# Kernel optimization log

Hardware: AMD Instinct MI355X
Metric: run time of the kernel (lower is better)

The kernel has to match this reference:

```python
import jax, jax.numpy as jnp
import numpy as np

N_NODES = 100000
N_EDGES = 3200000
IN_DIM = 128


def setup_inputs() -> dict:
    key = jax.random.key(0)
    ks = jax.random.split(key, 6)
    x = jax.random.normal(ks[0], (N_NODES, IN_DIM), dtype=jnp.float32)
    edge_index = jax.random.randint(ks[1], (2, N_EDGES), 0, N_NODES, dtype=jnp.int64)
    # Glorot-ish init for weights, zero bias (PyG GCNConv default has bias)
    W1 = jax.random.normal(ks[2], (IN_DIM, 32), dtype=jnp.float32) / np.sqrt(IN_DIM)
    b1 = jnp.zeros((32,), dtype=jnp.float32)
    W2 = jax.random.normal(ks[3], (32, 16), dtype=jnp.float32) / np.sqrt(32.0)
    b2 = jnp.zeros((16,), dtype=jnp.float32)
    Wf = jax.random.normal(ks[4], (16, 1), dtype=jnp.float32) / np.sqrt(16.0)
    bf = jnp.zeros((1,), dtype=jnp.float32)
    return {"x": x, "edge_index": edge_index, "W1": W1, "b1": b1,
            "W2": W2, "b2": b2, "Wf": Wf, "bf": bf}


def reference(x, edge_index, W1, b1, W2, b2, Wf, bf):
    N = x.shape[0]
    # PyG GCNConv: add self-loops, symmetric normalization D^-1/2 (A+I) D^-1/2
    loop = jnp.arange(N, dtype=edge_index.dtype)
    src = jnp.concatenate([edge_index[0], loop])  # message sources (x_j)
    dst = jnp.concatenate([edge_index[1], loop])  # aggregation targets
    deg = jax.ops.segment_sum(jnp.ones_like(dst, dtype=x.dtype), dst, num_segments=N)
    dinv = jax.lax.rsqrt(jnp.maximum(deg, 1.0))  # deg >= 1 due to self-loops
    norm = dinv[src] * dinv[dst]                  # per-edge coefficient

    def gcn_conv(h, W, b):
        h = h @ W                                 # linear transform first (small dim)
        msg = h[src] * norm[:, None]              # gather + scale
        return jax.ops.segment_sum(msg, dst, num_segments=N) + b  # scatter-add

    h = jax.nn.relu(gcn_conv(x, W1, b1))
    h = jax.nn.relu(gcn_conv(h, W2, b2))
    return (h @ Wf + bf).squeeze(-1)              # [N]
```

## Files before the change

### kernel.cpp

```cpp
#include <hip/hip_runtime.h>


#define TPB 256
#define NBUCK 512
#define BCAP 8192
#define CHUNK 8192

__device__ __forceinline__ unsigned f2bf(float f) {
    unsigned u = __float_as_uint(f);
    return (u + 0x7FFFu + ((u >> 16) & 1u)) >> 16;
}
__device__ __forceinline__ float bflo(unsigned u) { return __uint_as_float(u << 16); }
__device__ __forceinline__ float bfhi(unsigned u) { return __uint_as_float(u & 0xFFFF0000u); }

__global__ __launch_bounds__(512) void binA2_kernel(
        const int* __restrict__ src, const int* __restrict__ dst,
        int* __restrict__ bcur, unsigned* __restrict__ staging, int E, int NPB) {
    __shared__ unsigned packed[CHUNK];
    __shared__ unsigned short buckb[CHUNK];
    __shared__ int hist[NBUCK];
    __shared__ int scan_[NBUCK];
    __shared__ int lstart[NBUCK];
    __shared__ int lcur[NBUCK];
    __shared__ int gbase[NBUCK];
    int tid = threadIdx.x;
    int start = blockIdx.x * CHUNK;
    int sz = min(CHUNK, E - start);

    if (tid < NBUCK) hist[tid] = 0;
    __syncthreads();
    for (int i = tid; i < sz; i += 512) {
        unsigned d = (unsigned)dst[start + i];
        atomicAdd(&hist[d / (unsigned)NPB], 1);
    }
    __syncthreads();
    int v = (tid < NBUCK) ? hist[tid] : 0;
    if (tid < NBUCK) scan_[tid] = v;
    __syncthreads();
    for (int dd = 1; dd < NBUCK; dd <<= 1) {
        int t = 0;
        if (tid < NBUCK && tid >= dd) t = scan_[tid - dd];
        __syncthreads();
        if (tid < NBUCK) scan_[tid] += t;
        __syncthreads();
    }
    if (tid < NBUCK) {
        lstart[tid] = scan_[tid] - v;
        lcur[tid] = 0;
        gbase[tid] = atomicAdd(&bcur[tid], v);
    }
    __syncthreads();
    for (int i = tid; i < sz; i += 512) {
        unsigned d = (unsigned)dst[start + i];
        unsigned s = (unsigned)src[start + i];
        unsigned b = d / (unsigned)NPB;
        unsigned loc = d - b * (unsigned)NPB;
        int pos = atomicAdd(&lcur[b], 1);
        int si = lstart[b] + pos;
        packed[si] = (loc << 20) | s;
        buckb[si] = (unsigned short)b;
    }
    __syncthreads();
    for (int i = tid; i < sz; i += 512) {
        unsigned b = buckb[i];
        int dsti = gbase[b] + (i - lstart[b]);
        if (dsti < BCAP)
            staging[(size_t)b * BCAP + dsti] = packed[i];
    }
}

__global__ void buildB_kernel(const int* __restrict__ bcur,
                              const unsigned* __restrict__ staging,
                              int* __restrict__ offs, int* __restrict__ counts,
                              float* __restrict__ dinv, int* __restrict__ csr_src,
                              int N, int NPB) {
    __shared__ int sb[NBUCK];
    __shared__ int hist[512];
    __shared__ int scan_[512];
    __shared__ int cur[512];
    int b = blockIdx.x;
    int tid = threadIdx.x;
    if (tid < NBUCK) sb[tid] = min(bcur[tid], BCAP);
    __syncthreads();
    for (int d = 1; d < NBUCK; d <<= 1) {
        int t = 0;
        if (tid < NBUCK && tid >= d) t = sb[tid - d];
        __syncthreads();
        if (tid < NBUCK) sb[tid] += t;
        __syncthreads();
    }
    int sz = min(bcur[b], BCAP);
    int base = (b == 0) ? 0 : sb[b - 1];
    int n0 = b * NPB;
    int nn = min(NPB, N - n0);
    const unsigned* se = staging + (size_t)b * BCAP;

    hist[tid] = 0;
    __syncthreads();
    for (int i = tid; i < sz; i += 512)
        atomicAdd(&hist[se[i] >> 20], 1);
    __syncthreads();
    int h = hist[tid];
    scan_[tid] = h;
    __syncthreads();
    for (int d = 1; d < 512; d <<= 1) {
        int t = 0;
        if (tid >= d) t = scan_[tid - d];
        __syncthreads();
        scan_[tid] += t;
        __syncthreads();
    }
    int excl = scan_[tid] - h;
    cur[tid] = excl;
    if (tid < nn) {
        int node = n0 + tid;
        offs[node] = base + excl;
        counts[node] = h;
        dinv[node] = rsqrtf((float)(h + 1));
    }
    __syncthreads();
    for (int i = tid; i < sz; i += 512) {
        unsigned p = se[i];
        int pos = atomicAdd(&cur[p >> 20], 1);
        csr_src[base + pos] = (int)(p & 0xFFFFFu);
    }
}

__global__ __launch_bounds__(256) void gemm1_kernel(
        const float* __restrict__ x, const float* __restrict__ W1,
        const float* __restrict__ dinv, unsigned* __restrict__ xwd, int N) {
    __shared__ float ws_[128 * 32];
    for (int i = threadIdx.x; i < 128 * 32; i += 256) ws_[i] = W1[i];
    __syncthreads();
    int t = threadIdx.x;
    int jq = (t & 3) * 8;
    int n0 = blockIdx.x * 256 + (t >> 2) * 4;
    if (n0 >= N) return;
    int nc0 = min(n0 + 0, N - 1);
    int nc1 = min(n0 + 1, N - 1);
    int nc2 = min(n0 + 2, N - 1);
    int nc3 = min(n0 + 3, N - 1);
    const float4* xr0 = (const float4*)(x + (size_t)nc0 * 128);
    const float4* xr1 = (const float4*)(x + (size_t)nc1 * 128);
    const float4* xr2 = (const float4*)(x + (size_t)nc2 * 128);
    const float4* xr3 = (const float4*)(x + (size_t)nc3 * 128);
    float acc[4][8];
#pragma unroll
    for (int n = 0; n < 4; ++n)
#pragma unroll
        for (int j = 0; j < 8; ++j) acc[n][j] = 0.0f;
#pragma unroll 2
    for (int k4 = 0; k4 < 32; ++k4) {
        const float* wb = ws_ + (k4 * 4) * 32 + jq;
        float4 a0 = *(const float4*)(wb);
        float4 a1 = *(const float4*)(wb + 4);
        float4 b0 = *(const float4*)(wb + 32);
        float4 b1v = *(const float4*)(wb + 36);
        float4 c0 = *(const float4*)(wb + 64);
        float4 c1 = *(const float4*)(wb + 68);
        float4 d0 = *(const float4*)(wb + 96);
        float4 d1 = *(const float4*)(wb + 100);
        float4 xv0 = xr0[k4];
        float4 xv1 = xr1[k4];
        float4 xv2 = xr2[k4];
        float4 xv3 = xr3[k4];
#pragma unroll
        for (int n = 0; n < 4; ++n) {
            float4 xv = (n == 0) ? xv0 : (n == 1) ? xv1 : (n == 2) ? xv2 : xv3;
            acc[n][0] += xv.x * a0.x + xv.y * b0.x + xv.z * c0.x + xv.w * d0.x;
            acc[n][1] += xv.x * a0.y + xv.y * b0.y + xv.z * c0.y + xv.w * d0.y;
            acc[n][2] += xv.x * a0.z + xv.y * b0.z + xv.z * c0.z + xv.w * d0.z;
            acc[n][3] += xv.x * a0.w + xv.y * b0.w + xv.z * c0.w + xv.w * d0.w;
            acc[n][4] += xv.x * a1.x + xv.y * b1v.x + xv.z * c1.x + xv.w * d1.x;
            acc[n][5] += xv.x * a1.y + xv.y * b1v.y + xv.z * c1.y + xv.w * d1.y;
            acc[n][6] += xv.x * a1.z + xv.y * b1v.z + xv.z * c1.z + xv.w * d1.z;
            acc[n][7] += xv.x * a1.w + xv.y * b1v.w + xv.z * c1.w + xv.w * d1.w;
        }
    }
#pragma unroll
    for (int n = 0; n < 4; ++n) {
        int node = n0 + n;
        if (node >= N) break;
        float d = dinv[node];
        unsigned pk0 = f2bf(acc[n][0] * d) | (f2bf(acc[n][1] * d) << 16);
        unsigned pk1 = f2bf(acc[n][2] * d) | (f2bf(acc[n][3] * d) << 16);
        unsigned pk2 = f2bf(acc[n][4] * d) | (f2bf(acc[n][5] * d) << 16);
        unsigned pk3 = f2bf(acc[n][6] * d) | (f2bf(acc[n][7] * d) << 16);
        ((uint4*)(xwd + (size_t)node * 16))[t & 3] = make_uint4(pk0, pk1, pk2, pk3);
    }
}

__global__ __launch_bounds__(256) void aggF_kernel(
        const int* __restrict__ offs, const int* __restrict__ counts,
        const int* __restrict__ csr_src, const float* __restrict__ dinv,
        const unsigned* __restrict__ xwd, const float* __restrict__ b1,
        const float* __restrict__ W2, unsigned* __restrict__ h2wd, int N) {
    __shared__ float ws2[32 * 16];
    for (int i = threadIdx.x; i < 512; i += 256) ws2[i] = W2[i];
    __syncthreads();
    int t = threadIdx.x;
    int q = t & 3;
    int node = blockIdx.x * 64 + (t >> 2);
    if (node >= N) return;
    int off = offs[node];
    int deg = counts[node];
    float acc[8];
    {
        uint4 v = ((const uint4*)(xwd + (size_t)node * 16))[q];
        acc[0] = bflo(v.x); acc[1] = bfhi(v.x);
        acc[2] = bflo(v.y); acc[3] = bfhi(v.y);
        acc[4] = bflo(v.z); acc[5] = bfhi(v.z);
        acc[6] = bflo(v.w); acc[7] = bfhi(v.w);
    }
    int i = 0;
    for (; i + 1 < deg; i += 2) {
        int s0 = csr_src[off + i];
        int s1 = csr_src[off + i + 1];
        uint4 v0 = ((const uint4*)(xwd + (size_t)s0 * 16))[q];
        uint4 v1 = ((const uint4*)(xwd + (size_t)s1 * 16))[q];
        acc[0] += bflo(v0.x) + bflo(v1.x); acc[1] += bfhi(v0.x) + bfhi(v1.x);
        acc[2] += bflo(v0.y) + bflo(v1.y); acc[3] += bfhi(v0.y) + bfhi(v1.y);
        acc[4] += bflo(v0.z) + bflo(v1.z); acc[5] += bfhi(v0.z) + bfhi(v1.z);
        acc[6] += bflo(v0.w) + bflo(v1.w); acc[7] += bfhi(v0.w) + bfhi(v1.w);
    }
    if (i < deg) {
        int s = csr_src[off + i];
        uint4 v = ((const uint4*)(xwd + (size_t)s * 16))[q];
        acc[0] += bflo(v.x); acc[1] += bfhi(v.x);
        acc[2] += bflo(v.y); acc[3] += bfhi(v.y);
        acc[4] += bflo(v.z); acc[5] += bfhi(v.z);
        acc[6] += bflo(v.w); acc[7] += bfhi(v.w);
    }
    float dv = dinv[node];
    float part[16];
#pragma unroll
    for (int j = 0; j < 16; ++j) part[j] = 0.0f;
    const float* bq = b1 + q * 8;
#pragma unroll
    for (int k = 0; k < 8; ++k) {
        float h = fmaxf(acc[k] * dv + bq[k], 0.0f);
        const float* wr = ws2 + (q * 8 + k) * 16;
        float4 w0 = *(const float4*)(wr);
        float4 w1 = *(const float4*)(wr + 4);
        float4 w2 = *(const float4*)(wr + 8);
        float4 w3 = *(const float4*)(wr + 12);
        part[0]  += h * w0.x; part[1]  += h * w0.y; part[2]  += h * w0.z; part[3]  += h * w0.w;
        part[4]  += h * w1.x; part[5]  += h * w1.y; part[6]  += h * w1.z; part[7]  += h * w1.w;
        part[8]  += h * w2.x; part[9]  += h * w2.y; part[10] += h * w2.z; part[11] += h * w2.w;
        part[12] += h * w3.x; part[13] += h * w3.y; part[14] += h * w3.z; part[15] += h * w3.w;
    }
    float p8[8];
#pragma unroll
    for (int j = 0; j < 8; ++j) {
        float send = (q & 1) ? part[j] : part[j + 8];
        float keep = (q & 1) ? part[j + 8] : part[j];
        p8[j] = keep + __shfl_xor(send, 1, 64);
    }
    float p4[4];
#pragma unroll
    for (int j = 0; j < 4; ++j) {
        float send = (q & 2) ? p8[j] : p8[j + 4];
        float keep = (q & 2) ? p8[j + 4] : p8[j];
        p4[j] = keep + __shfl_xor(send, 2, 64);
    }
    unsigned pk0 = f2bf(p4[0] * dv) | (f2bf(p4[1] * dv) << 16);
    unsigned pk1 = f2bf(p4[2] * dv) | (f2bf(p4[3] * dv) << 16);
    int slot = ((q & 1) << 1) | ((q >> 1) & 1);
    ((uint2*)(h2wd + (size_t)node * 8))[slot] = make_uint2(pk0, pk1);
}

__global__ __launch_bounds__(256) void aggS16f_kernel(
        const int* __restrict__ offs, const int* __restrict__ counts,
        const int* __restrict__ csr_src, const float* __restrict__ dinv,
        const unsigned* __restrict__ h2wd,
        const float* __restrict__ b2, const float* __restrict__ Wf,
        const float* __restrict__ bf, float* __restrict__ out, int N) {
    __shared__ float bs_[16];
    __shared__ float wf_[16];
    __shared__ float bfv;
    int t = threadIdx.x;
    if (t < 16) { bs_[t] = b2[t]; wf_[t] = Wf[t]; }
    if (t == 0) bfv = bf[0];
    __syncthreads();
    int q = t & 1;
    int node = blockIdx.x * 128 + (t >> 1);
    if (node >= N) return;
    int off = offs[node];
    int deg = counts[node];
    float acc[8];
    {
        uint4 v = ((const uint4*)(h2wd + (size_t)node * 8))[q];
        acc[0] = bflo(v.x); acc[1] = bfhi(v.x);
        acc[2] = bflo(v.y); acc[3] = bfhi(v.y);
        acc[4] = bflo(v.z); acc[5] = bfhi(v.z);
        acc[6] = bflo(v.w); acc[7] = bfhi(v.w);
    }
    int i = 0;
    for (; i + 1 < deg; i += 2) {
        int s0 = csr_src[off + i];
        int s1 = csr_src[off + i + 1];
        uint4 v0 = ((const uint4*)(h2wd + (size_t)s0 * 8))[q];
        uint4 v1 = ((const uint4*)(h2wd + (size_t)s1 * 8))[q];
        acc[0] += bflo(v0.x) + bflo(v1.x); acc[1] += bfhi(v0.x) + bfhi(v1.x);
        acc[2] += bflo(v0.y) + bflo(v1.y); acc[3] += bfhi(v0.y) + bfhi(v1.y);
        acc[4] += bflo(v0.z) + bflo(v1.z); acc[5] += bfhi(v0.z) + bfhi(v1.z);
        acc[6] += bflo(v0.w) + bflo(v1.w); acc[7] += bfhi(v0.w) + bfhi(v1.w);
    }
    if (i < deg) {
        int s = csr_src[off + i];
        uint4 v = ((const uint4*)(h2wd + (size_t)s * 8))[q];
        acc[0] += bflo(v.x); acc[1] += bfhi(v.x);
        acc[2] += bflo(v.y); acc[3] += bfhi(v.y);
        acc[4] += bflo(v.z); acc[5] += bfhi(v.z);
        acc[6] += bflo(v.w); acc[7] += bfhi(v.w);
    }
    float dv = dinv[node];
    const float* bq = bs_ + q * 8;
    const float* wq = wf_ + q * 8;
    float part = 0.f;
#pragma unroll
    for (int k = 0; k < 8; ++k)
        part += fmaxf(acc[k] * dv + bq[k], 0.f) * wq[k];
    part += __shfl_xor(part, 1, 64);
    if (q == 0) out[node] = part + bfv;
}

extern "C" void kernel_launch(void* const* d_in, const int* in_sizes, int n_in,
                              void* d_out, int out_size, void* d_ws, size_t ws_size,
                              hipStream_t stream) {
    const float* x  = (const float*)d_in[0];
    const int*   ei = (const int*)d_in[1];
    const float* W1 = (const float*)d_in[2];
    const float* b1 = (const float*)d_in[3];
    const float* W2 = (const float*)d_in[4];
    const float* b2 = (const float*)d_in[5];
    const float* Wf = (const float*)d_in[6];
    const float* bf = (const float*)d_in[7];

    int N = in_sizes[0] / 128;
    int E = in_sizes[1] / 2;
    const int* src = ei;
    const int* dst = ei + E;
    int NPB = (N + NBUCK - 1) / NBUCK;

    size_t Np = ((size_t)N + 3) & ~(size_t)3;
    size_t Ep = ((size_t)E + 3) & ~(size_t)3;
    int* wsI      = (int*)d_ws;
    int* counts   = wsI;
    int* offs     = counts + Np;
    int* bcur     = offs + Np;
    int* csr_src  = bcur + NBUCK;
    float* dinv   = (float*)(csr_src + Ep);
    unsigned* xwd = (unsigned*)(dinv + Np);
    unsigned* staging = xwd + 16 * Np;
    unsigned* h2wd = staging;
    float* out    = (float*)d_out;

    int nbG1 = (N + 255) / 256;
    int nbC  = (E + CHUNK - 1) / CHUNK;
    int nbA32 = (N + 63) / 64;
    int nbA16 = (N + 127) / 128;

    hipMemsetAsync(bcur, 0, NBUCK * sizeof(int), stream);
    binA2_kernel<<<nbC, 512, 0, stream>>>(src, dst, bcur, staging, E, NPB);
    buildB_kernel<<<NBUCK, 512, 0, stream>>>(bcur, staging, offs, counts,
                                             dinv, csr_src, N, NPB);
    gemm1_kernel<<<nbG1, 256, 0, stream>>>(x, W1, dinv, xwd, N);
    aggF_kernel<<<nbA32, 256, 0, stream>>>(offs, counts, csr_src, dinv, xwd,
                                           b1, W2, h2wd, N);
    aggS16f_kernel<<<nbA16, 256, 0, stream>>>(offs, counts, csr_src, dinv, h2wd,
                                              b2, Wf, bf, out, N);
}
```

Measured before the change: 259.6 us.

## Aggregate directly from destination buckets with shared-memory atomics, dropping CSR build

Result: slower. 1.004 ms (+286.6%).

```diff
diff --git a/kernel.cpp b/kernel.cpp
--- a/kernel.cpp
+++ b/kernel.cpp
@@ -1,10 +1,10 @@
 #include <hip/hip_runtime.h>
 
 
-#define TPB 256
 #define NBUCK 512
 #define BCAP 8192
-#define CHUNK 8192
+#define CHUNK 4096
+#define NPBMAX 256
 
 __device__ __forceinline__ unsigned f2bf(float f) {
     unsigned u = __float_as_uint(f);
@@ -27,37 +27,45 @@
     int start = blockIdx.x * CHUNK;
     int sz = min(CHUNK, E - start);
 
-    if (tid < NBUCK) hist[tid] = 0;
-    __syncthreads();
-    for (int i = tid; i < sz; i += 512) {
-        unsigned d = (unsigned)dst[start + i];
-        atomicAdd(&hist[d / (unsigned)NPB], 1);
-    }
-    __syncthreads();
-    int v = (tid < NBUCK) ? hist[tid] : 0;
-    if (tid < NBUCK) scan_[tid] = v;
+    unsigned dreg[8], sreg[8];
+    hist[tid] = 0;
+#pragma unroll
+    for (int c = 0; c < 8; ++c) {
+        int i = tid + c * 512;
+        if (i < sz) {
+            dreg[c] = (unsigned)dst[start + i];
+            sreg[c] = (unsigned)src[start + i];
+        } else {
+            dreg[c] = 0xFFFFFFFFu;
+        }
+    }
+    __syncthreads();
+#pragma unroll
+    for (int c = 0; c < 8; ++c)
+        if (dreg[c] != 0xFFFFFFFFu) atomicAdd(&hist[dreg[c] / (unsigned)NPB], 1);
+    __syncthreads();
+    int v = hist[tid];
+    scan_[tid] = v;
     __syncthreads();
     for (int dd = 1; dd < NBUCK; dd <<= 1) {
-        int t = 0;
-        if (tid < NBUCK && tid >= dd) t = scan_[tid - dd];
+        int t = (tid >= dd) ? scan_[tid - dd] : 0;
         __syncthreads();
-        if (tid < NBUCK) scan_[tid] += t;
+        scan_[tid] += t;
         __syncthreads();
     }
-    if (tid < NBUCK) {
-        lstart[tid] = scan_[tid] - v;
-        lcur[tid] = 0;
-        gbase[tid] = atomicAdd(&bcur[tid], v);
-    }
-    __syncthreads();
-    for (int i = tid; i < sz; i += 512) {
-        unsigned d = (unsigned)dst[start + i];
-        unsigned s = (unsigned)src[start + i];
+    lstart[tid] = scan_[tid] - v;
+    lcur[tid] = 0;
+    gbase[tid] = atomicAdd(&bcur[tid], v);
+    __syncthreads();
+#pragma unroll
+    for (int c = 0; c < 8; ++c) {
+        if (dreg[c] == 0xFFFFFFFFu) continue;
+        unsigned d = dreg[c];
         unsigned b = d / (unsigned)NPB;
         unsigned loc = d - b * (unsigned)NPB;
         int pos = atomicAdd(&lcur[b], 1);
         int si = lstart[b] + pos;
-        packed[si] = (loc << 20) | s;
+        packed[si] = (loc << 20) | sreg[c];
         buckb[si] = (unsigned short)b;
     }
     __syncthreads();
@@ -69,61 +77,22 @@
     }
 }
 
-__global__ void buildB_kernel(const int* __restrict__ bcur,
-                              const unsigned* __restrict__ staging,
-                              int* __restrict__ offs, int* __restrict__ counts,
-                              float* __restrict__ dinv, int* __restrict__ csr_src,
-                              int N, int NPB) {
-    __shared__ int sb[NBUCK];
-    __shared__ int hist[512];
-    __shared__ int scan_[512];
-    __shared__ int cur[512];
+__global__ __launch_bounds__(512) void countB_kernel(
+        const int* __restrict__ bcur, const unsigned* __restrict__ staging,
+        float* __restrict__ dinv, int N, int NPB) {
+    __shared__ int hist[NPBMAX];
     int b = blockIdx.x;
     int tid = threadIdx.x;
-    if (tid < NBUCK) sb[tid] = min(bcur[tid], BCAP);
-    __syncthreads();
-    for (int d = 1; d < NBUCK; d <<= 1) {
-        int t = 0;
-        if (tid < NBUCK && tid >= d) t = sb[tid - d];
-        __syncthreads();
-        if (tid < NBUCK) sb[tid] += t;
-        __syncthreads();
-    }
+    if (tid < NPBMAX) hist[tid] = 0;
+    __syncthreads();
     int sz = min(bcur[b], BCAP);
-    int base = (b == 0) ? 0 : sb[b - 1];
-    int n0 = b * NPB;
-    int nn = min(NPB, N - n0);
     const unsigned* se = staging + (size_t)b * BCAP;
-
-    hist[tid] = 0;
-    __syncthreads();
     for (int i = tid; i < sz; i += 512)
         atomicAdd(&hist[se[i] >> 20], 1);
     __syncthreads();
-    int h = hist[tid];
-    scan_[tid] = h;
-    __syncthreads();
-    for (int d = 1; d < 512; d <<= 1) {
-        int t = 0;
-        if (tid >= d) t = scan_[tid - d];
-        __syncthreads();
-        scan_[tid] += t;
-        __syncthreads();
-    }
-    int excl = scan_[tid] - h;
-    cur[tid] = excl;
-    if (tid < nn) {
-        int node = n0 + tid;
-        offs[node] = base + excl;
-        counts[node] = h;
-        dinv[node] = rsqrtf((float)(h + 1));
-    }
-    __syncthreads();
-    for (int i = tid; i < sz; i += 512) {
-        unsigned p = se[i];
-        int pos = atomicAdd(&cur[p >> 20], 1);
-        csr_src[base + pos] = (int)(p & 0xFFFFFu);
-    }
+    int n0 = b * NPB;
+    if (tid < NPB && n0 + tid < N)
+        dinv[n0 + tid] = rsqrtf((float)(hist[tid] + 1));
 }
 
 __global__ __launch_bounds__(256) void gemm1_kernel(
@@ -190,139 +159,121 @@
     }
 }
 
-__global__ __launch_bounds__(256) void aggF_kernel(
-        const int* __restrict__ offs, const int* __restrict__ counts,
-        const int* __restrict__ csr_src, const float* __restrict__ dinv,
-        const unsigned* __restrict__ xwd, const float* __restrict__ b1,
-        const float* __restrict__ W2, unsigned* __restrict__ h2wd, int N) {
+__global__ __launch_bounds__(512) void aggB1_kernel(
+        const int* __restrict__ bcur, const unsigned* __restrict__ staging,
+        const float* __restrict__ dinv, const unsigned* __restrict__ xwd,
+        const float* __restrict__ b1, const float* __restrict__ W2,
+        unsigned* __restrict__ h2wd, int N, int NPB) {
+    __shared__ float acc[NPBMAX * 33];
     __shared__ float ws2[32 * 16];
-    for (int i = threadIdx.x; i < 512; i += 256) ws2[i] = W2[i];
-    __syncthreads();
-    int t = threadIdx.x;
-    int q = t & 3;
-    int node = blockIdx.x * 64 + (t >> 2);
-    if (node >= N) return;
-    int off = offs[node];
-    int deg = counts[node];
-    float acc[8];
-    {
-        uint4 v = ((const uint4*)(xwd + (size_t)node * 16))[q];
-        acc[0] = bflo(v.x); acc[1] = bfhi(v.x);
-        acc[2] = bflo(v.y); acc[3] = bfhi(v.y);
-        acc[4] = bflo(v.z); acc[5] = bfhi(v.z);
-        acc[6] = bflo(v.w); acc[7] = bfhi(v.w);
-    }
-    int i = 0;
-    for (; i + 1 < deg; i += 2) {
-        int s0 = csr_src[off + i];
-        int s1 = csr_src[off + i + 1];
-        uint4 v0 = ((const uint4*)(xwd + (size_t)s0 * 16))[q];
-        uint4 v1 = ((const uint4*)(xwd + (size_t)s1 * 16))[q];
-        acc[0] += bflo(v0.x) + bflo(v1.x); acc[1] += bfhi(v0.x) + bfhi(v1.x);
-        acc[2] += bflo(v0.y) + bflo(v1.y); acc[3] += bfhi(v0.y) + bfhi(v1.y);
-        acc[4] += bflo(v0.z) + bflo(v1.z); acc[5] += bfhi(v0.z) + bfhi(v1.z);
-        acc[6] += bflo(v0.w) + bflo(v1.w); acc[7] += bfhi(v0.w) + bfhi(v1.w);
-    }
-    if (i < deg) {
-        int s = csr_src[off + i];
+    __shared__ float bs1[32];
+    int b = blockIdx.x;
+    int tid = threadIdx.x;
+    int n0 = b * NPB;
+    int nn = min(NPB, N - n0);
+    if (nn <= 0) return;
+    if (tid < 512) ws2[tid] = W2[tid];
+    if (tid < 32) bs1[tid] = b1[tid];
+    for (int i = tid; i < nn * 4; i += 512) {
+        int loc = i >> 2, q = i & 3;
+        uint4 v = ((const uint4*)(xwd + (size_t)(n0 + loc) * 16))[q];
+        float* a = acc + loc * 33 + q * 8;
+        a[0] = bflo(v.x); a[1] = bfhi(v.x);
+        a[2] = bflo(v.y); a[3] = bfhi(v.y);
+        a[4] = bflo(v.z); a[5] = bfhi(v.z);
+        a[6] = bflo(v.w); a[7] = bfhi(v.w);
+    }
+    __syncthreads();
+    int sz = min(bcur[b], BCAP);
+    const unsigned* se = staging + (size_t)b * BCAP;
+    int q = tid & 3;
+    for (int e = tid >> 2; e < sz; e += 128) {
+        unsigned p = se[e];
+        int loc = p >> 20;
+        int s = (int)(p & 0xFFFFFu);
         uint4 v = ((const uint4*)(xwd + (size_t)s * 16))[q];
-        acc[0] += bflo(v.x); acc[1] += bfhi(v.x);
-        acc[2] += bflo(v.y); acc[3] += bfhi(v.y);
-        acc[4] += bflo(v.z); acc[5] += bfhi(v.z);
-        acc[6] += bflo(v.w); acc[7] += bfhi(v.w);
-    }
-    float dv = dinv[node];
-    float part[16];
-#pragma unroll
-    for (int j = 0; j < 16; ++j) part[j] = 0.0f;
-    const float* bq = b1 + q * 8;
-#pragma unroll
-    for (int k = 0; k < 8; ++k) {
-        float h = fmaxf(acc[k] * dv + bq[k], 0.0f);
-        const float* wr = ws2 + (q * 8 + k) * 16;
-        float4 w0 = *(const float4*)(wr);
-        float4 w1 = *(const float4*)(wr + 4);
-        float4 w2 = *(const float4*)(wr + 8);
-        float4 w3 = *(const float4*)(wr + 12);
-        part[0]  += h * w0.x; part[1]  += h * w0.y; part[2]  += h * w0.z; part[3]  += h * w0.w;
-        part[4]  += h * w1.x; part[5]  += h * w1.y; part[6]  += h * w1.z; part[7]  += h * w1.w;
-        part[8]  += h * w2.x; part[9]  += h * w2.y; part[10] += h * w2.z; part[11] += h * w2.w;
-        part[12] += h * w3.x; part[13] += h * w3.y; part[14] += h * w3.z; part[15] += h * w3.w;
-    }
-    float p8[8];
-#pragma unroll
-    for (int j = 0; j < 8; ++j) {
-        float send = (q & 1) ? part[j] : part[j + 8];
-        float keep = (q & 1) ? part[j + 8] : part[j];
-        p8[j] = keep + __shfl_xor(send, 1, 64);
-    }
-    float p4[4];
-#pragma unroll
-    for (int j = 0; j < 4; ++j) {
-        float send = (q & 2) ? p8[j] : p8[j + 4];
-        float keep = (q & 2) ? p8[j + 4] : p8[j];
-        p4[j] = keep + __shfl_xor(send, 2, 64);
-    }
-    unsigned pk0 = f2bf(p4[0] * dv) | (f2bf(p4[1] * dv) << 16);
-    unsigned pk1 = f2bf(p4[2] * dv) | (f2bf(p4[3] * dv) << 16);
-    int slot = ((q & 1) << 1) | ((q >> 1) & 1);
-    ((uint2*)(h2wd + (size_t)node * 8))[slot] = make_uint2(pk0, pk1);
-}
-
-__global__ __launch_bounds__(256) void aggS16f_kernel(
-        const int* __restrict__ offs, const int* __restrict__ counts,
-        const int* __restrict__ csr_src, const float* __restrict__ dinv,
-        const unsigned* __restrict__ h2wd,
+        float* a = acc + loc * 33 + q * 8;
+        atomicAdd(&a[0], bflo(v.x)); atomicAdd(&a[1], bfhi(v.x));
+        atomicAdd(&a[2], bflo(v.y)); atomicAdd(&a[3], bfhi(v.y));
+        atomicAdd(&a[4], bflo(v.z)); atomicAdd(&a[5], bfhi(v.z));
+        atomicAdd(&a[6], bflo(v.w)); atomicAdd(&a[7], bfhi(v.w));
+    }
+    __syncthreads();
+    for (int loc = tid; loc < nn; loc += 512) {
+        int node = n0 + loc;
+        float dv = dinv[node];
+        const float* a = acc + loc * 33;
+        float h[32];
+#pragma unroll
+        for (int k = 0; k < 32; ++k) h[k] = fmaxf(a[k] * dv + bs1[k], 0.0f);
+        float o[16];
+#pragma unroll
+        for (int j = 0; j < 16; ++j) o[j] = 0.0f;
+#pragma unroll
+        for (int k = 0; k < 32; ++k) {
+            float hv = h[k];
+#pragma unroll
+            for (int j = 0; j < 16; ++j) o[j] += hv * ws2[k * 16 + j];
+        }
+        unsigned pk[8];
+#pragma unroll
+        for (int j = 0; j < 8; ++j)
+            pk[j] = f2bf(o[2 * j] * dv) | (f2bf(o[2 * j + 1] * dv) << 16);
+        uint4* hp = (uint4*)(h2wd + (size_t)node * 8);
+        hp[0] = make_uint4(pk[0], pk[1], pk[2], pk[3]);
+        hp[1] = make_uint4(pk[4], pk[5], pk[6], pk[7]);
+    }
+}
+
+__global__ __launch_bounds__(512) void aggB2_kernel(
+        const int* __restrict__ bcur, const unsigned* __restrict__ staging,
+        const float* __restrict__ dinv, const unsigned* __restrict__ h2wd,
         const float* __restrict__ b2, const float* __restrict__ Wf,
-        const float* __restrict__ bf, float* __restrict__ out, int N) {
-    __shared__ float bs_[16];
-    __shared__ float wf_[16];
-    __shared__ float bfv;
-    int t = threadIdx.x;
-    if (t < 16) { bs_[t] = b2[t]; wf_[t] = Wf[t]; }
-    if (t == 0) bfv = bf[0];
-    __syncthreads();
-    int q = t & 1;
-    int node = blockIdx.x * 128 + (t >> 1);
-    if (node >= N) return;
-    int off = offs[node];
-    int deg = counts[node];
-    float acc[8];
-    {
-        uint4 v = ((const uint4*)(h2wd + (size_t)node * 8))[q];
-        acc[0] = bflo(v.x); acc[1] = bfhi(v.x);
-        acc[2] = bflo(v.y); acc[3] = bfhi(v.y);
-        acc[4] = bflo(v.z); acc[5] = bfhi(v.z);
-        acc[6] = bflo(v.w); acc[7] = bfhi(v.w);
-    }
-    int i = 0;
-    for (; i + 1 < deg; i += 2) {
-        int s0 = csr_src[off + i];
-        int s1 = csr_src[off + i + 1];
-        uint4 v0 = ((const uint4*)(h2wd + (size_t)s0 * 8))[q];
-        uint4 v1 = ((const uint4*)(h2wd + (size_t)s1 * 8))[q];
-        acc[0] += bflo(v0.x) + bflo(v1.x); acc[1] += bfhi(v0.x) + bfhi(v1.x);
-        acc[2] += bflo(v0.y) + bflo(v1.y); acc[3] += bfhi(v0.y) + bfhi(v1.y);
-        acc[4] += bflo(v0.z) + bflo(v1.z); acc[5] += bfhi(v0.z) + bfhi(v1.z);
-        acc[6] += bflo(v0.w) + bflo(v1.w); acc[7] += bfhi(v0.w) + bfhi(v1.w);
-    }
-    if (i < deg) {
-        int s = csr_src[off + i];
+        const float* __restrict__ bfp, float* __restrict__ out, int N, int NPB) {
+    __shared__ float acc[NPBMAX * 17];
+    __shared__ float bs2[16];
+    __shared__ float wf[16];
+    int b = blockIdx.x;
+    int tid = threadIdx.x;
+    int n0 = b * NPB;
+    int nn = min(NPB, N - n0);
+    if (nn <= 0) return;
+    if (tid < 16) { bs2[tid] = b2[tid]; wf[tid] = Wf[tid]; }
+    for (int i = tid; i < nn * 2; i += 512) {
+        int loc = i >> 1, q = i & 1;
+        uint4 v = ((const uint4*)(h2wd + (size_t)(n0 + loc) * 8))[q];
+        float* a = acc + loc * 17 + q * 8;
+        a[0] = bflo(v.x); a[1] = bfhi(v.x);
+        a[2] = bflo(v.y); a[3] = bfhi(v.y);
+        a[4] = bflo(v.z); a[5] = bfhi(v.z);
+        a[6] = bflo(v.w); a[7] = bfhi(v.w);
+    }
+    __syncthreads();
+    int sz = min(bcur[b], BCAP);
+    const unsigned* se = staging + (size_t)b * BCAP;
+    int q = tid & 1;
+    for (int e = tid >> 1; e < sz; e += 256) {
+        unsigned p = se[e];
+        int loc = p >> 20;
+        int s = (int)(p & 0xFFFFFu);
         uint4 v = ((const uint4*)(h2wd + (size_t)s * 8))[q];
-        acc[0] += bflo(v.x); acc[1] += bfhi(v.x);
-        acc[2] += bflo(v.y); acc[3] += bfhi(v.y);
-        acc[4] += bflo(v.z); acc[5] += bfhi(v.z);
-        acc[6] += bflo(v.w); acc[7] += bfhi(v.w);
-    }
-    float dv = dinv[node];
-    const float* bq = bs_ + q * 8;
-    const float* wq = wf_ + q * 8;
-    float part = 0.f;
-#pragma unroll
-    for (int k = 0; k < 8; ++k)
-        part += fmaxf(acc[k] * dv + bq[k], 0.f) * wq[k];
-    part += __shfl_xor(part, 1, 64);
-    if (q == 0) out[node] = part + bfv;
+        float* a = acc + loc * 17 + q * 8;
+        atomicAdd(&a[0], bflo(v.x)); atomicAdd(&a[1], bfhi(v.x));
+        atomicAdd(&a[2], bflo(v.y)); atomicAdd(&a[3], bfhi(v.y));
+        atomicAdd(&a[4], bflo(v.z)); atomicAdd(&a[5], bfhi(v.z));
+        atomicAdd(&a[6], bflo(v.w)); atomicAdd(&a[7], bfhi(v.w));
+    }
+    __syncthreads();
+    for (int loc = tid; loc < nn; loc += 512) {
+        int node = n0 + loc;
+        float dv = dinv[node];
+        const float* a = acc + loc * 17;
+        float part = 0.0f;
+#pragma unroll
+        for (int k = 0; k < 16; ++k)
+            part += fmaxf(a[k] * dv + bs2[k], 0.0f) * wf[k];
+        out[node] = part + bfp[0];
+    }
 }
 
 extern "C" void kernel_launch(void* const* d_in, const int* in_sizes, int n_in,
@@ -344,30 +295,22 @@
     int NPB = (N + NBUCK - 1) / NBUCK;
 
     size_t Np = ((size_t)N + 3) & ~(size_t)3;
-    size_t Ep = ((size_t)E + 3) & ~(size_t)3;
-    int* wsI      = (int*)d_ws;
-    int* counts   = wsI;
-    int* offs     = counts + Np;
-    int* bcur     = offs + Np;
-    int* csr_src  = bcur + NBUCK;
-    float* dinv   = (float*)(csr_src + Ep);
-    unsigned* xwd = (unsigned*)(dinv + Np);
-    unsigned* staging = xwd + 16 * Np;
-    unsigned* h2wd = staging;
-    float* out    = (float*)d_out;
-
+    int* bcur        = (int*)d_ws;
+    float* dinv      = (float*)(bcur + NBUCK);
+    unsigned* xwd    = (unsigned*)(dinv + Np);
+    unsigned* h2wd   = xwd + 16 * Np;
+    unsigned* staging= h2wd + 8 * Np;
+    float* out       = (float*)d_out;
+
+    int nbC  = (E + CHUNK - 1) / CHUNK;
     int nbG1 = (N + 255) / 256;
-    int nbC  = (E + CHUNK - 1) / CHUNK;
-    int nbA32 = (N + 63) / 64;
-    int nbA16 = (N + 127) / 128;
 
     hipMemsetAsync(bcur, 0, NBUCK * sizeof(int), stream);
     binA2_kernel<<<nbC, 512, 0, stream>>>(src, dst, bcur, staging, E, NPB);
-    buildB_kernel<<<NBUCK, 512, 0, stream>>>(bcur, staging, offs, counts,
-                                             dinv, csr_src, N, NPB);
+    countB_kernel<<<NBUCK, 512, 0, stream>>>(bcur, staging, dinv, N, NPB);
     gemm1_kernel<<<nbG1, 256, 0, stream>>>(x, W1, dinv, xwd, N);
-    aggF_kernel<<<nbA32, 256, 0, stream>>>(offs, counts, csr_src, dinv, xwd,
-                                           b1, W2, h2wd, N);
-    aggS16f_kernel<<<nbA16, 256, 0, stream>>>(offs, counts, csr_src, dinv, h2wd,
-                                              b2, Wf, bf, out, N);
-}
+    aggB1_kernel<<<NBUCK, 512, 0, stream>>>(bcur, staging, dinv, xwd,
+                                            b1, W2, h2wd, N, NPB);
+    aggB2_kernel<<<NBUCK, 512, 0, stream>>>(bcur, staging, dinv, h2wd,
+                                            b2, Wf, bf, out, N, NPB);
+}
```

## Replace bucketed two-pass CSR build with global atomic count, scan, scatter

Applied to the files above, without the earlier changes.

Measured after the change: 616.8 us. 138% more time.

```diff
diff --git a/kernel.cpp b/kernel.cpp
--- a/kernel.cpp
+++ b/kernel.cpp
@@ -2,9 +2,6 @@
 
 
 #define TPB 256
-#define NBUCK 512
-#define BCAP 8192
-#define CHUNK 8192
 
 __device__ __forceinline__ unsigned f2bf(float f) {
     unsigned u = __float_as_uint(f);
@@ -13,116 +10,69 @@
 __device__ __forceinline__ float bflo(unsigned u) { return __uint_as_float(u << 16); }
 __device__ __forceinline__ float bfhi(unsigned u) { return __uint_as_float(u & 0xFFFF0000u); }
 
-__global__ __launch_bounds__(512) void binA2_kernel(
+__global__ __launch_bounds__(256) void countA_kernel(
+        const int* __restrict__ dst, int* __restrict__ counts, int E) {
+    int stride = gridDim.x * 256;
+    for (int i = blockIdx.x * 256 + threadIdx.x; i < E; i += stride)
+        atomicAdd(&counts[dst[i]], 1);
+}
+
+__global__ __launch_bounds__(512) void scan1_kernel(
+        const int* __restrict__ counts, int* __restrict__ offs,
+        int* __restrict__ bsum, float* __restrict__ dinv, int N) {
+    __shared__ int s[512];
+    int tid = threadIdx.x;
+    int g = blockIdx.x * 512 + tid;
+    int c = (g < N) ? counts[g] : 0;
+    s[tid] = c;
+    __syncthreads();
+    for (int d = 1; d < 512; d <<= 1) {
+        int t = (tid >= d) ? s[tid - d] : 0;
+        __syncthreads();
+        s[tid] += t;
+        __syncthreads();
+    }
+    if (g < N) {
+        offs[g] = s[tid] - c;
+        dinv[g] = rsqrtf((float)(c + 1));
+    }
+    if (tid == 511) bsum[blockIdx.x] = s[511];
+}
+
+__global__ __launch_bounds__(512) void scan2_kernel(int* __restrict__ bsum, int nb) {
+    __shared__ int s[512];
+    int tid = threadIdx.x;
+    int v = (tid < nb) ? bsum[tid] : 0;
+    s[tid] = v;
+    __syncthreads();
+    for (int d = 1; d < 512; d <<= 1) {
+        int t = (tid >= d) ? s[tid - d] : 0;
+        __syncthreads();
+        s[tid] += t;
+        __syncthreads();
+    }
+    if (tid < nb) bsum[tid] = s[tid] - v;
+}
+
+__global__ __launch_bounds__(256) void scan3_kernel(
+        int* __restrict__ offs, const int* __restrict__ bsum,
+        int* __restrict__ cursor, int N) {
+    int g = blockIdx.x * 256 + threadIdx.x;
+    if (g < N) {
+        int o = offs[g] + bsum[g >> 9];
+        offs[g] = o;
+        cursor[g] = o;
+    }
+}
+
+__global__ __launch_bounds__(256) void scatter_kernel(
         const int* __restrict__ src, const int* __restrict__ dst,
-        int* __restrict__ bcur, unsigned* __restrict__ staging, int E, int NPB) {
-    __shared__ unsigned packed[CHUNK];
-    __shared__ unsigned short buckb[CHUNK];
-    __shared__ int hist[NBUCK];
-    __shared__ int scan_[NBUCK];
-    __shared__ int lstart[NBUCK];
-    __shared__ int lcur[NBUCK];
-    __shared__ int gbase[NBUCK];
-    int tid = threadIdx.x;
-    int start = blockIdx.x * CHUNK;
-    int sz = min(CHUNK, E - start);
-
-    if (tid < NBUCK) hist[tid] = 0;
-    __syncthreads();
-    for (int i = tid; i < sz; i += 512) {
-        unsigned d = (unsigned)dst[start + i];
-        atomicAdd(&hist[d / (unsigned)NPB], 1);
-    }
-    __syncthreads();
-    int v = (tid < NBUCK) ? hist[tid] : 0;
-    if (tid < NBUCK) scan_[tid] = v;
-    __syncthreads();
-    for (int dd = 1; dd < NBUCK; dd <<= 1) {
-        int t = 0;
-        if (tid < NBUCK && tid >= dd) t = scan_[tid - dd];
-        __syncthreads();
-        if (tid < NBUCK) scan_[tid] += t;
-        __syncthreads();
-    }
-    if (tid < NBUCK) {
-        lstart[tid] = scan_[tid] - v;
-        lcur[tid] = 0;
-        gbase[tid] = atomicAdd(&bcur[tid], v);
-    }
-    __syncthreads();
-    for (int i = tid; i < sz; i += 512) {
-        unsigned d = (unsigned)dst[start + i];
-        unsigned s = (unsigned)src[start + i];
-        unsigned b = d / (unsigned)NPB;
-        unsigned loc = d - b * (unsigned)NPB;
-        int pos = atomicAdd(&lcur[b], 1);
-        int si = lstart[b] + pos;
-        packed[si] = (loc << 20) | s;
-        buckb[si] = (unsigned short)b;
-    }
-    __syncthreads();
-    for (int i = tid; i < sz; i += 512) {
-        unsigned b = buckb[i];
-        int dsti = gbase[b] + (i - lstart[b]);
-        if (dsti < BCAP)
-            staging[(size_t)b * BCAP + dsti] = packed[i];
-    }
-}
-
-__global__ void buildB_kernel(const int* __restrict__ bcur,
-                              const unsigned* __restrict__ staging,
-                              int* __restrict__ offs, int* __restrict__ counts,
-                              float* __restrict__ dinv, int* __restrict__ csr_src,
-                              int N, int NPB) {
-    __shared__ int sb[NBUCK];
-    __shared__ int hist[512];
-    __shared__ int scan_[512];
-    __shared__ int cur[512];
-    int b = blockIdx.x;
-    int tid = threadIdx.x;
-    if (tid < NBUCK) sb[tid] = min(bcur[tid], BCAP);
-    __syncthreads();
-    for (int d = 1; d < NBUCK; d <<= 1) {
-        int t = 0;
-        if (tid < NBUCK && tid >= d) t = sb[tid - d];
-        __syncthreads();
-        if (tid < NBUCK) sb[tid] += t;
-        __syncthreads();
-    }
-    int sz = min(bcur[b], BCAP);
-    int base = (b == 0) ? 0 : sb[b - 1];
-    int n0 = b * NPB;
-    int nn = min(NPB, N - n0);
-    const unsigned* se = staging + (size_t)b * BCAP;
-
-    hist[tid] = 0;
-    __syncthreads();
-    for (int i = tid; i < sz; i += 512)
-        atomicAdd(&hist[se[i] >> 20], 1);
-    __syncthreads();
-    int h = hist[tid];
-    scan_[tid] = h;
-    __syncthreads();
-    for (int d = 1; d < 512; d <<= 1) {
-        int t = 0;
-        if (tid >= d) t = scan_[tid - d];
-        __syncthreads();
-        scan_[tid] += t;
-        __syncthreads();
-    }
-    int excl = scan_[tid] - h;
-    cur[tid] = excl;
-    if (tid < nn) {
-        int node = n0 + tid;
-        offs[node] = base + excl;
-        counts[node] = h;
-        dinv[node] = rsqrtf((float)(h + 1));
-    }
-    __syncthreads();
-    for (int i = tid; i < sz; i += 512) {
-        unsigned p = se[i];
-        int pos = atomicAdd(&cur[p >> 20], 1);
-        csr_src[base + pos] = (int)(p & 0xFFFFFu);
+        int* __restrict__ cursor, int* __restrict__ csr_src, int E) {
+    int stride = gridDim.x * 256;
+    for (int i = blockIdx.x * 256 + threadIdx.x; i < E; i += stride) {
+        int d = dst[i];
+        int pos = atomicAdd(&cursor[d], 1);
+        csr_src[pos] = src[i];
     }
 }
 
@@ -341,30 +291,32 @@
     int E = in_sizes[1] / 2;
     const int* src = ei;
     const int* dst = ei + E;
-    int NPB = (N + NBUCK - 1) / NBUCK;
 
     size_t Np = ((size_t)N + 3) & ~(size_t)3;
     size_t Ep = ((size_t)E + 3) & ~(size_t)3;
-    int* wsI      = (int*)d_ws;
-    int* counts   = wsI;
+    int* counts   = (int*)d_ws;
     int* offs     = counts + Np;
-    int* bcur     = offs + Np;
-    int* csr_src  = bcur + NBUCK;
+    int* cursor   = offs + Np;
+    int* bsum     = cursor + Np;
+    int* csr_src  = bsum + 512;
     float* dinv   = (float*)(csr_src + Ep);
     unsigned* xwd = (unsigned*)(dinv + Np);
-    unsigned* staging = xwd + 16 * Np;
-    unsigned* h2wd = staging;
+    unsigned* h2wd= xwd + 16 * Np;
     float* out    = (float*)d_out;
 
+    int nbE  = min((E + 255) / 256, 2048);
+    int nbS1 = (N + 511) / 512;
+    int nbN  = (N + 255) / 256;
     int nbG1 = (N + 255) / 256;
-    int nbC  = (E + CHUNK - 1) / CHUNK;
     int nbA32 = (N + 63) / 64;
     int nbA16 = (N + 127) / 128;
 
-    hipMemsetAsync(bcur, 0, NBUCK * sizeof(int), stream);
-    binA2_kernel<<<nbC, 512, 0, stream>>>(src, dst, bcur, staging, E, NPB);
-    buildB_kernel<<<NBUCK, 512, 0, stream>>>(bcur, staging, offs, counts,
-                                             dinv, csr_src, N, NPB);
+    hipMemsetAsync(counts, 0, Np * sizeof(int), stream);
+    countA_kernel<<<nbE, 256, 0, stream>>>(dst, counts, E);
+    scan1_kernel<<<nbS1, 512, 0, stream>>>(counts, offs, bsum, dinv, N);
+    scan2_kernel<<<1, 512, 0, stream>>>(bsum, nbS1);
+    scan3_kernel<<<nbN, 256, 0, stream>>>(offs, bsum, cursor, N);
+    scatter_kernel<<<nbE, 256, 0, stream>>>(src, dst, cursor, csr_src, E);
     gemm1_kernel<<<nbG1, 256, 0, stream>>>(x, W1, dinv, xwd, N);
     aggF_kernel<<<nbA32, 256, 0, stream>>>(offs, counts, csr_src, dinv, xwd,
                                            b1, W2, h2wd, N);
```
